# Kernel optimization log

Hardware: AMD Instinct MI355X
Metric: run time of the kernel (lower is better)

## Reference

```python
import jax, jax.numpy as jnp
import numpy as np

T, IN, MEM, OUT = 4096, 1024, 1024, 1024


def setup_inputs() -> dict:
    key = jax.random.key(0)
    ks = jax.random.split(key, 16)
    def mat(k, o, i):
        # xavier-like scale
        return jax.random.normal(k, (o, i), jnp.float32) / np.float32(np.sqrt(i))
    inp = {"x": jax.random.normal(ks[0], (T, IN), jnp.float32)}
    idx = 1
    for side in ("l", "r"):
        for g in ("f", "i", "c"):
            inp[f"w{g}_{side}"] = mat(ks[idx], MEM, IN)
            inp[f"u{g}_{side}"] = mat(jax.random.fold_in(ks[idx], 1), MEM, MEM)
            inp[f"b{g}_{side}"] = jnp.zeros((MEM,), jnp.float32)
            idx += 1
    inp["wo"] = mat(ks[idx], OUT, MEM)
    inp["uo"] = mat(ks[idx + 1], OUT, MEM)
    inp["bo"] = jnp.zeros((OUT,), jnp.float32)
    inp["c0_l"] = jnp.zeros((MEM,), jnp.float32)
    inp["c0_r"] = jnp.zeros((MEM,), jnp.float32)
    return inp


def _gated_scan(x, wf, uf, bf, wi, ui, bi, wc, uc, bc, c0):
    """Runs the EnvLSTM gated recurrence; returns stack of PRE-update cell states
    (the original appends _c to the env list BEFORE updating it)."""
    def step(c, xt):
        f = jax.nn.sigmoid(wf @ xt + uf @ c + bf)
        i = jax.nn.sigmoid(wi @ xt + ui @ c + bi)
        g = jnp.tanh(wc @ xt + uc @ c + bc)
        return f * c + i * g, c
    _, env = jax.lax.scan(step, c0, x)
    return env  # [T, MEM]


def reference(x,
              wf_l, uf_l, bf_l, wi_l, ui_l, bi_l, wc_l, uc_l, bc_l,
              wf_r, uf_r, bf_r, wi_r, ui_r, bi_r, wc_r, uc_r, bc_r,
              wo, uo, bo, c0_l, c0_r):
    # Left (forward-time) scan: Lenv[i] = cell state before consuming x[i]
    lenv = _gated_scan(x, wf_l, uf_l, bf_l, wi_l, ui_l, bi_l, wc_l, uc_l, bc_l, c0_l)
    # Right scan over reversed time; Renv_rev[k] = state before consuming x[T-1-k].
    renv_rev = _gated_scan(x[::-1], wf_r, uf_r, bf_r, wi_r, ui_r, bi_r, wc_r, uc_r, bc_r, c0_r)
    # Original output step uses Renv[T-1-i], i.e. the reversed-scan pre-state
    # aligned back to time order:
    renv = renv_rev[::-1]
    # oNN with lev=0: tanh(Wo @ Lenv[i] + Uo @ Renv_aligned[i] + bo), vectorized.
    out = jnp.tanh(jnp.einsum("tm,om->to", lenv, wo)
                   + jnp.einsum("tm,om->to", renv, uo) + bo)
    return out  # [T, OUT] (original returns a list of these vectors)
```

## Files before the change

### kernel.cpp

```cpp
#include <hip/hip_runtime.h>
#include <hip/hip_bf16.h>


typedef __attribute__((ext_vector_type(4))) float f32x4;

static constexpr int TSEQ = 4096;

struct Ptr6 { const float* p[6]; };

__device__ inline void atomic_store_f64(double* p, double v) {
  __hip_atomic_store((unsigned long long*)p,
                     __builtin_bit_cast(unsigned long long, v),
                     __ATOMIC_RELAXED, __HIP_MEMORY_SCOPE_AGENT);
}
__device__ inline double atomic_load_f64(double* p) {
  unsigned long long u = __hip_atomic_load((unsigned long long*)p,
                                           __ATOMIC_RELAXED, __HIP_MEMORY_SCOPE_AGENT);
  return __builtin_bit_cast(double, u);
}

__global__ void init_k(const float* __restrict__ c0l, const float* __restrict__ c0r,
                       double* __restrict__ cslots, int* __restrict__ flags,
                       float* __restrict__ env) {
  int tid = blockIdx.x * blockDim.x + threadIdx.x;
  if (tid < 1024) {
    double v = (double)c0l[tid];
    cslots[tid] = v;
    env[tid] = (float)v;
  } else if (tid < 2048) {
    int j = tid - 1024;
    double v = (double)c0r[j];
    cslots[2048 + j] = v;
    env[(size_t)(TSEQ - 1) * 2048 + 1024 + j] = (float)v;
  }
  if (tid < 256) flags[tid] = 0;
}

__global__ __launch_bounds__(256) void gemm_f64v_k(
    const float* __restrict__ A, Ptr6 B, Ptr6 BIAS,
    float* __restrict__ CH, __hip_bfloat16* __restrict__ CL) {
  __shared__ double As[16][66];
  __shared__ double Bs[16][66];
  const int tid = threadIdx.x;
  const int m0 = blockIdx.y * 64, n0 = blockIdx.x * 64;
  const int tx = tid & 15, ty = tid >> 4;
  const int lrow = tid >> 2, lkq = tid & 3;
  const float* bmat = B.p[n0 >> 10] + (size_t)(n0 & 1023) * 1024;

  double acc[4][4] = {};

  for (int k0 = 0; k0 < 1024; k0 += 16) {
    f32x4 va = *(const f32x4*)(A + (size_t)(m0 + lrow) * 1024 + k0 + lkq * 4);
    f32x4 vb = *(const f32x4*)(bmat + (size_t)lrow * 1024 + k0 + lkq * 4);
    __syncthreads();
#pragma unroll
    for (int e = 0; e < 4; ++e) {
      As[lkq * 4 + e][lrow] = (double)va[e];
      Bs[lkq * 4 + e][lrow] = (double)vb[e];
    }
    __syncthreads();
#pragma unroll
    for (int k = 0; k < 16; ++k) {
      double a[4], b[4];
#pragma unroll
      for (int i = 0; i < 4; ++i) a[i] = As[k][ty + 16 * i];
#pragma unroll
      for (int jj = 0; jj < 4; ++jj) b[jj] = Bs[k][tx + 16 * jj];
#pragma unroll
      for (int i = 0; i < 4; ++i)
#pragma unroll
        for (int jj = 0; jj < 4; ++jj)
          acc[i][jj] = fma(a[i], b[jj], acc[i][jj]);
    }
  }

#pragma unroll
  for (int i = 0; i < 4; ++i)
#pragma unroll
    for (int jj = 0; jj < 4; ++jj) {
      int row = m0 + ty + 16 * i;
      int col = n0 + tx + 16 * jj;
      double s = acc[i][jj] + (double)BIAS.p[col >> 10][col & 1023];
      size_t idx = (size_t)row * 6144 + col;
      float hi = (float)s;
      CH[idx] = hi;
      CL[idx] = __float2bfloat16((float)(s - (double)hi));
    }
}

__global__ __launch_bounds__(512, 2) void recur_k(
    const float* __restrict__ u0, const float* __restrict__ u1, const float* __restrict__ u2,
    const float* __restrict__ u3, const float* __restrict__ u4, const float* __restrict__ u5,
    const float* __restrict__ WxH,
    const __hip_bfloat16* __restrict__ WxL,
    double* __restrict__ cslots,
    int* __restrict__ flags,
    float* __restrict__ env)
{
  const int bid = blockIdx.x;
  const int dir = bid >> 7;
  const int wg  = bid & 127;
  const int tid = threadIdx.x;
  const int wave = tid >> 6;
  const int lane = tid & 63;
  const int j = wg * 8 + wave;

  const float* Uf = dir ? u3 : u0;
  const float* Ui = dir ? u4 : u1;
  const float* Uc = dir ? u5 : u2;

  double wf[16], wi[16], wcc[16];
#pragma unroll
  for (int q = 0; q < 16; ++q) {
    const size_t idx = (size_t)j * 1024 + q * 64 + lane;
    wf[q] = (double)Uf[idx]; wi[q] = (double)Ui[idx]; wcc[q] = (double)Uc[idx];
  }

  __shared__ double cl[1024];
  double* slot = cslots + dir * 2048;
  int* fl = flags + dir * 128;
  const size_t wxoff = (size_t)dir * 3072 + j;
  float* envp = env + dir * 1024 + j;

  for (int t = 0; t < TSEQ - 1; ++t) {
    const int xr = dir ? (TSEQ - 1 - t) : t;
    const size_t base = (size_t)xr * 6144 + wxoff;
    const double wxf = (double)WxH[base] + (double)__bfloat162float(WxL[base]);
    const double wxi = (double)WxH[base + 1024] + (double)__bfloat162float(WxL[base + 1024]);
    const double wxg = (double)WxH[base + 2048] + (double)__bfloat162float(WxL[base + 2048]);

    if (tid < 128) {
      while (__hip_atomic_load(&fl[tid], __ATOMIC_RELAXED, __HIP_MEMORY_SCOPE_AGENT) < t)
        __builtin_amdgcn_s_sleep(1);
    }
    __syncthreads();

    {
      double* src = slot + (size_t)(t & 1) * 1024 + 2 * tid;
      const double a = atomic_load_f64(src);
      const double b = atomic_load_f64(src + 1);
      cl[2 * tid] = a;
      cl[2 * tid + 1] = b;
    }
    __syncthreads();

    const double cold = cl[j];
    double sf = 0.0, si = 0.0, sg = 0.0;
#pragma unroll
    for (int q = 0; q < 16; ++q) {
      const double cc = cl[q * 64 + lane];
      sf = fma(wf[q], cc, sf);
      si = fma(wi[q], cc, si);
      sg = fma(wcc[q], cc, sg);
    }
#pragma unroll
    for (int off = 1; off < 64; off <<= 1) {
      sf += __shfl_xor(sf, off);
      si += __shfl_xor(si, off);
      sg += __shfl_xor(sg, off);
    }

    const double af = sf + wxf, ai = si + wxi, ag = sg + wxg;
    const double fgate = 1.0 / (1.0 + exp(-af));
    const double igate = 1.0 / (1.0 + exp(-ai));
    const double ggate = tanh(ag);
    const double cn = fgate * cold + igate * ggate;

    if (lane == 0) {
      atomic_store_f64(&slot[(size_t)((t + 1) & 1) * 1024 + j], cn);
      const int er = dir ? (TSEQ - 2 - t) : (t + 1);
      envp[(size_t)er * 2048] = (float)cn;
    }
    __syncthreads();
    if (tid == 0)
      __hip_atomic_store(&fl[wg], t + 1, __ATOMIC_RELAXED, __HIP_MEMORY_SCOPE_AGENT);
  }
}

__global__ __launch_bounds__(256) void gemm_out_f64_k(
    const float* __restrict__ A, const float* __restrict__ wo,
    const float* __restrict__ uo, const float* __restrict__ bo,
    float* __restrict__ C) {
  __shared__ double As[16][66];
  __shared__ double Bs[16][66];
  const int tid = threadIdx.x;
  const int m0 = blockIdx.y * 64, n0 = blockIdx.x * 64;
  const int tx = tid & 15, ty = tid >> 4;
  const int lrow = tid >> 2, lkq = tid & 3;

  double acc[4][4] = {};

  for (int k0 = 0; k0 < 2048; k0 += 16) {
    f32x4 va = *(const f32x4*)(A + (size_t)(m0 + lrow) * 2048 + k0 + lkq * 4);
    const float* bsrc = (k0 < 1024)
        ? wo + (size_t)(n0 + lrow) * 1024 + k0 + lkq * 4
        : uo + (size_t)(n0 + lrow) * 1024 + (k0 - 1024) + lkq * 4;
    f32x4 vb = *(const f32x4*)bsrc;
    __syncthreads();
#pragma unroll
    for (int e = 0; e < 4; ++e) {
      As[lkq * 4 + e][lrow] = (double)va[e];
      Bs[lkq * 4 + e][lrow] = (double)vb[e];
    }
    __syncthreads();
#pragma unroll
    for (int k = 0; k < 16; ++k) {
      double a[4], b[4];
#pragma unroll
      for (int i = 0; i < 4; ++i) a[i] = As[k][ty + 16 * i];
#pragma unroll
      for (int jj = 0; jj < 4; ++jj) b[jj] = Bs[k][tx + 16 * jj];
#pragma unroll
      for (int i = 0; i < 4; ++i)
#pragma unroll
        for (int jj = 0; jj < 4; ++jj)
          acc[i][jj] = fma(a[i], b[jj], acc[i][jj]);
    }
  }

#pragma unroll
  for (int i = 0; i < 4; ++i)
#pragma unroll
    for (int jj = 0; jj < 4; ++jj) {
      int row = m0 + ty + 16 * i;
      int col = n0 + tx + 16 * jj;
      double s = acc[i][jj] + (double)bo[col];
      C[(size_t)row * 1024 + col] = (float)tanh(s);
    }
}

extern "C" void kernel_launch(void* const* d_in, const int* in_sizes, int n_in,
                              void* d_out, int out_size, void* d_ws, size_t ws_size,
                              hipStream_t stream) {
  if (n_in < 24) return;
  const float* x    = (const float*)d_in[0];
  const float* wf_l = (const float*)d_in[1];
  const float* uf_l = (const float*)d_in[2];
  const float* bf_l = (const float*)d_in[3];
  const float* wi_l = (const float*)d_in[4];
  const float* ui_l = (const float*)d_in[5];
  const float* bi_l = (const float*)d_in[6];
  const float* wc_l = (const float*)d_in[7];
  const float* uc_l = (const float*)d_in[8];
  const float* bc_l = (const float*)d_in[9];
  const float* wf_r = (const float*)d_in[10];
  const float* uf_r = (const float*)d_in[11];
  const float* bf_r = (const float*)d_in[12];
  const float* wi_r = (const float*)d_in[13];
  const float* ui_r = (const float*)d_in[14];
  const float* bi_r = (const float*)d_in[15];
  const float* wc_r = (const float*)d_in[16];
  const float* uc_r = (const float*)d_in[17];
  const float* bc_r = (const float*)d_in[18];
  const float* wo   = (const float*)d_in[19];
  const float* uo   = (const float*)d_in[20];
  const float* bo   = (const float*)d_in[21];
  const float* c0l  = (const float*)d_in[22];
  const float* c0r  = (const float*)d_in[23];

  const size_t NWX = (size_t)TSEQ * 6144;
  char* p = (char*)d_ws;
  auto carve = [&](size_t bytes) -> char* {
    char* r = p; p += (bytes + 255) & ~(size_t)255; return r;
  };
  float*          WxH  = (float*)carve(NWX * 4);
  __hip_bfloat16* WxL  = (__hip_bfloat16*)carve(NWX * 2);
  float*          envc = (float*)carve((size_t)TSEQ * 2048 * 4);
  double*         cslots = (double*)carve(4096 * 8);
  int*            flags  = (int*)carve(256 * 4);
  if ((size_t)(p - (char*)d_ws) > ws_size) return;

  init_k<<<8, 256, 0, stream>>>(c0l, c0r, cslots, flags, envc);

  Ptr6 Bw{{wf_l, wi_l, wc_l, wf_r, wi_r, wc_r}};
  Ptr6 Bb{{bf_l, bi_l, bc_l, bf_r, bi_r, bc_r}};
  gemm_f64v_k<<<dim3(96, 64), 256, 0, stream>>>(x, Bw, Bb, WxH, WxL);

  recur_k<<<256, 512, 0, stream>>>(uf_l, ui_l, uc_l, uf_r, ui_r, uc_r,
                                   WxH, WxL, cslots, flags, envc);

  gemm_out_f64_k<<<dim3(16, 64), 256, 0, stream>>>(envc, wo, uo, bo, (float*)d_out);
}
```

Baseline: 23.79 ms.

## Replace per-block flag barrier with step-tagged data words in recurrence exchange

The cross-block handoff of cell states in the persistent recurrence kernel no longer uses separate per-workgroup flags plus two barriers. Each double is split into two 64-bit words whose upper halves carry the step number, so readers spin directly on the data until all tags match. This removes the flag write, one __syncthreads per step and the serialized flag poll, and shared memory is double-buffered so the trailing barrier can go. In exchange every thread polls four atomic words per step, which doubles the exchange traffic and adds more L2 polling pressure.

New measurement: 31.53 ms. 32.5% more time.

```diff
diff --git a/kernel.cpp b/kernel.cpp
--- a/kernel.cpp
+++ b/kernel.cpp
@@ -5,35 +5,32 @@
 typedef __attribute__((ext_vector_type(4))) float f32x4;
 
 static constexpr int TSEQ = 4096;
+typedef unsigned long long ull;
 
 struct Ptr6 { const float* p[6]; };
 
-__device__ inline void atomic_store_f64(double* p, double v) {
-  __hip_atomic_store((unsigned long long*)p,
-                     __builtin_bit_cast(unsigned long long, v),
-                     __ATOMIC_RELAXED, __HIP_MEMORY_SCOPE_AGENT);
-}
-__device__ inline double atomic_load_f64(double* p) {
-  unsigned long long u = __hip_atomic_load((unsigned long long*)p,
-                                           __ATOMIC_RELAXED, __HIP_MEMORY_SCOPE_AGENT);
-  return __builtin_bit_cast(double, u);
-}
+__device__ inline void atomic_store_u64(ull* p, ull v) {
+  __hip_atomic_store(p, v, __ATOMIC_RELAXED, __HIP_MEMORY_SCOPE_AGENT);
+}
+__device__ inline ull atomic_load_u64(ull* p) {
+  return __hip_atomic_load(p, __ATOMIC_RELAXED, __HIP_MEMORY_SCOPE_AGENT);
+}
+
 
 __global__ void init_k(const float* __restrict__ c0l, const float* __restrict__ c0r,
-                       double* __restrict__ cslots, int* __restrict__ flags,
-                       float* __restrict__ env) {
+                       ull* __restrict__ comm, float* __restrict__ env) {
   int tid = blockIdx.x * blockDim.x + threadIdx.x;
-  if (tid < 1024) {
-    double v = (double)c0l[tid];
-    cslots[tid] = v;
-    env[tid] = (float)v;
-  } else if (tid < 2048) {
-    int j = tid - 1024;
-    double v = (double)c0r[j];
-    cslots[2048 + j] = v;
-    env[(size_t)(TSEQ - 1) * 2048 + 1024 + j] = (float)v;
-  }
-  if (tid < 256) flags[tid] = 0;
+  if (tid >= 2048) return;
+  const int dirv = tid >> 10, j = tid & 1023;
+  const double v = (double)(dirv ? c0r[j] : c0l[j]);
+  const ull bits = __builtin_bit_cast(ull, v);
+  ull* base = comm + (size_t)dirv * 4096;
+  atomic_store_u64(&base[2 * j], bits & 0xffffffffull);
+  atomic_store_u64(&base[2 * j + 1], bits >> 32);
+  atomic_store_u64(&base[2048 + 2 * j], 0xFFFFFFFF00000000ull);
+  atomic_store_u64(&base[2048 + 2 * j + 1], 0xFFFFFFFF00000000ull);
+  if (dirv == 0) env[j] = (float)v;
+  else env[(size_t)(TSEQ - 1) * 2048 + 1024 + j] = (float)v;
 }
 
 __global__ __launch_bounds__(256) void gemm_f64v_k(
@@ -93,8 +90,7 @@
     const float* __restrict__ u3, const float* __restrict__ u4, const float* __restrict__ u5,
     const float* __restrict__ WxH,
     const __hip_bfloat16* __restrict__ WxL,
-    double* __restrict__ cslots,
-    int* __restrict__ flags,
+    ull* __restrict__ comm,
     float* __restrict__ env)
 {
   const int bid = blockIdx.x;
@@ -116,11 +112,10 @@
     wf[q] = (double)Uf[idx]; wi[q] = (double)Ui[idx]; wcc[q] = (double)Uc[idx];
   }
 
-  __shared__ double cl[1024];
-  double* slot = cslots + dir * 2048;
-  int* fl = flags + dir * 128;
+  __shared__ double cl[2][1024];
   const size_t wxoff = (size_t)dir * 3072 + j;
   float* envp = env + dir * 1024 + j;
+  ull* commd = comm + (size_t)dir * 4096;
 
   for (int t = 0; t < TSEQ - 1; ++t) {
     const int xr = dir ? (TSEQ - 1 - t) : t;
@@ -129,26 +124,33 @@
     const double wxi = (double)WxH[base + 1024] + (double)__bfloat162float(WxL[base + 1024]);
     const double wxg = (double)WxH[base + 2048] + (double)__bfloat162float(WxL[base + 2048]);
 
-    if (tid < 128) {
-      while (__hip_atomic_load(&fl[tid], __ATOMIC_RELAXED, __HIP_MEMORY_SCOPE_AGENT) < t)
+    {
+      ull* src = commd + (size_t)(t & 1) * 2048 + 4 * tid;
+      const unsigned want = (unsigned)t;
+      ull w0, w1, w2, w3;
+      for (;;) {
+        w0 = atomic_load_u64(src);
+        w1 = atomic_load_u64(src + 1);
+        w2 = atomic_load_u64(src + 2);
+        w3 = atomic_load_u64(src + 3);
+        if ((unsigned)(w0 >> 32) == want && (unsigned)(w1 >> 32) == want &&
+            (unsigned)(w2 >> 32) == want && (unsigned)(w3 >> 32) == want)
+          break;
         __builtin_amdgcn_s_sleep(1);
-    }
-    __syncthreads();
-
-    {
-      double* src = slot + (size_t)(t & 1) * 1024 + 2 * tid;
-      const double a = atomic_load_f64(src);
-      const double b = atomic_load_f64(src + 1);
-      cl[2 * tid] = a;
-      cl[2 * tid + 1] = b;
-    }
-    __syncthreads();
-
-    const double cold = cl[j];
+      }
+      cl[t & 1][2 * tid] =
+          __builtin_bit_cast(double, (w0 & 0xffffffffull) | (w1 << 32));
+      cl[t & 1][2 * tid + 1] =
+          __builtin_bit_cast(double, (w2 & 0xffffffffull) | (w3 << 32));
+    }
+    __syncthreads();
+
+    const double* c = cl[t & 1];
+    const double cold = c[j];
     double sf = 0.0, si = 0.0, sg = 0.0;
 #pragma unroll
     for (int q = 0; q < 16; ++q) {
-      const double cc = cl[q * 64 + lane];
+      const double cc = c[q * 64 + lane];
       sf = fma(wf[q], cc, sf);
       si = fma(wi[q], cc, si);
       sg = fma(wcc[q], cc, sg);
@@ -167,13 +169,14 @@
     const double cn = fgate * cold + igate * ggate;
 
     if (lane == 0) {
-      atomic_store_f64(&slot[(size_t)((t + 1) & 1) * 1024 + j], cn);
+      const ull bits = __builtin_bit_cast(ull, cn);
+      const ull tag = (ull)(unsigned)(t + 1) << 32;
+      ull* dst = commd + (size_t)((t + 1) & 1) * 2048 + (size_t)j * 2;
+      atomic_store_u64(dst, (bits & 0xffffffffull) | tag);
+      atomic_store_u64(dst + 1, (bits >> 32) | tag);
       const int er = dir ? (TSEQ - 2 - t) : (t + 1);
       envp[(size_t)er * 2048] = (float)cn;
     }
-    __syncthreads();
-    if (tid == 0)
-      __hip_atomic_store(&fl[wg], t + 1, __ATOMIC_RELAXED, __HIP_MEMORY_SCOPE_AGENT);
   }
 }
 
@@ -266,18 +269,17 @@
   float*          WxH  = (float*)carve(NWX * 4);
   __hip_bfloat16* WxL  = (__hip_bfloat16*)carve(NWX * 2);
   float*          envc = (float*)carve((size_t)TSEQ * 2048 * 4);
-  double*         cslots = (double*)carve(4096 * 8);
-  int*            flags  = (int*)carve(256 * 4);
+  ull*            comm = (ull*)carve(8192 * 8);
   if ((size_t)(p - (char*)d_ws) > ws_size) return;
 
-  init_k<<<8, 256, 0, stream>>>(c0l, c0r, cslots, flags, envc);
+  init_k<<<8, 256, 0, stream>>>(c0l, c0r, comm, envc);
 
   Ptr6 Bw{{wf_l, wi_l, wc_l, wf_r, wi_r, wc_r}};
   Ptr6 Bb{{bf_l, bi_l, bc_l, bf_r, bi_r, bc_r}};
   gemm_f64v_k<<<dim3(96, 64), 256, 0, stream>>>(x, Bw, Bb, WxH, WxL);
 
   recur_k<<<256, 512, 0, stream>>>(uf_l, ui_l, uc_l, uf_r, ui_r, uc_r,
-                                   WxH, WxL, cslots, flags, envc);
+                                   WxH, WxL, comm, envc);
 
   gemm_out_f64_k<<<dim3(16, 64), 256, 0, stream>>>(envc, wo, uo, bo, (float*)d_out);
 }
```
